# Kernel tuning notes

Measured on AMD Instinct MI355X. Metric: run time of the kernel, lower is better.

The kernel has to match this reference:

```python
import jax, jax.numpy as jnp
import numpy as np

B, T, D, H, HS = 4, 1024, 1024, 16, 64
DW, DA, DG, DV = 64, 64, 128, 32
DM = H * HS  # == D here
EPS = 1e-5
DECAY_C = -0.606531  # -exp(-0.5)


def setup_inputs() -> dict:
    key = jax.random.key(0)
    ks = jax.random.split(key, 24)
    n = lambda k, s: jax.random.normal(k, s, dtype=jnp.float32)
    w = lambda k, s: n(k, s) * (1.0 / np.sqrt(s[0]))
    return dict(
        current=n(ks[0], (B, T, D)),
        prev=n(ks[1], (B, T, D)),
        v_first=n(ks[2], (B, T, DM)),
        rwkvag=jax.random.uniform(ks[3], (6, D), dtype=jnp.float32),
        rw_W=w(ks[4], (D, D)),
        w1=w(ks[5], (D, DW)), w2=w(ks[6], (DW, DM)), w2_b=n(ks[7], (DM,)) * 0.1,
        kw_W=w(ks[8], (D, DM)), vw_W=w(ks[9], (D, DM)),
        a1=w(ks[10], (D, DA)), a2=w(ks[11], (DA, DM)), a2_b=n(ks[12], (DM,)) * 0.1,
        v1=w(ks[13], (D, DV)), v2=w(ks[14], (DV, DM)), v2_b=n(ks[15], (DM,)) * 0.1,
        g1=w(ks[16], (D, DG)), g2=w(ks[17], (DG, DM)), g2_b=n(ks[18], (DM,)) * 0.1,
        k_k=jnp.ones((DM,)), k_a=jax.random.uniform(ks[19], (DM,), dtype=jnp.float32),
        r_k=jnp.ones((DM,)),
        gn_scale=jnp.ones((DM,)), gn_bias=jnp.zeros((DM,)),
        out_W=w(ks[20], (DM, D)),
    )


def _add_heads(x):
    return x.reshape(x.shape[:-1] + (H, HS))


def reference(current, prev, v_first, rwkvag, rw_W, w1, w2, w2_b, kw_W, vw_W,
              a1, a2, a2_b, v1, v2, v2_b, g1, g2, g2_b,
              k_k, k_a, r_k, gn_scale, gn_bias, out_W):
    diff = prev - current
    # per-channel token-shift mixing for the 6 branches: (B,T,6,D)
    x6 = current[..., None, :] + rwkvag * diff[..., None, :]
    xr, xw, xk, xv, xa, xg = (x6[..., i, :] for i in range(6))

    r = xr @ rw_W
    wl = jnp.tanh(xw @ w1) @ w2 + w2_b          # w-LoRA (tanh, bias_post)
    k = xk @ kw_W
    v = xv @ vw_W
    a = jax.nn.sigmoid((xa @ a1) @ a2 + a2_b)   # a-LoRA (bias_post) + sigmoid
    g = jax.nn.sigmoid(xg @ g1) @ g2 + g2_b     # g-LoRA (sigmoid act)

    kk = _add_heads(k * k_k)
    kk = kk / jnp.linalg.norm(kk, axis=-1, keepdims=True)
    k = k * (1.0 + (a - 1.0) * k_a)
    v = v + (v_first - v) * jax.nn.sigmoid((xv @ v1) @ v2 + v2_b)
    wdec = jnp.exp(DECAY_C * jax.nn.sigmoid(wl))  # decay in (exp(-0.6065), 1)

    rk_sum = _add_heads(r * k * r_k).sum(-1, keepdims=True)  # (B,T,H,1)
    rh, wh, kh, vh = _add_heads(r), _add_heads(wdec), _add_heads(k), _add_heads(v)
    at = -kk
    bt = kk * _add_heads(a)

    def step(state, xs):
        rt, wt, ktt, vt, att, btt = xs  # each (B,H,HS)
        sa = jnp.einsum('bhvk,bhk->bhv', state, att)
        state = (state * wt[:, :, None, :]
                 + sa[..., None] * btt[:, :, None, :]
                 + vt[..., None] * ktt[:, :, None, :])
        y = jnp.einsum('bhvk,bhk->bhv', state, rt)
        return state, y

    xs = tuple(jnp.moveaxis(x, 1, 0) for x in (rh, wh, kh, vh, at, bt))
    state0 = jnp.zeros((B, H, HS, HS), dtype=current.dtype)
    state, ys = jax.lax.scan(step, state0, xs)
    out = jnp.moveaxis(ys, 0, 1)  # (B,T,H,HS)

    # GroupNorm with n_head groups (normalize within each head)
    mu = out.mean(-1, keepdims=True)
    var = out.var(-1, keepdims=True)
    outn = (out - mu) * jax.lax.rsqrt(var + EPS)
    outn = outn.reshape(B, T, DM) * gn_scale + gn_bias

    outn = outn + (rk_sum * vh).reshape(B, T, DM)
    y = (outn * g) @ out_W
    return y, state, v_first
```

## Files before the change

### kernel.cpp

```cpp
#include <hip/hip_runtime.h>
#include <math.h>

#define NT 4096
#define DD 1024
#define NH 16
#define HSZ 64
#define GN_EPS 1e-5f
#define DECAY_C -0.606531f

typedef __attribute__((ext_vector_type(8))) short short8;
typedef __attribute__((ext_vector_type(4))) float float4v;

#define GLB(p) ((const __attribute__((address_space(1))) void*)(p))
#define LDS(p) ((__attribute__((address_space(3))) void*)(p))

#define MEMFENCE asm volatile("" ::: "memory")

__device__ __forceinline__ float sigm(float x) { return 1.f / (1.f + __expf(-x)); }

__device__ __forceinline__ unsigned short f2bf(float f) {
    unsigned int u = __float_as_uint(f);
    u = (u + 0x7fffu + ((u >> 16) & 1u)) >> 16;
    return (unsigned short)u;
}
__device__ __forceinline__ float bf2f(unsigned short h) {
    return __uint_as_float(((unsigned int)h) << 16);
}

__device__ __forceinline__ float row_sum16(float x) {
    int t;
    t = __builtin_amdgcn_update_dpp(0, __float_as_int(x), 0x128, 0xF, 0xF, true);
    x += __int_as_float(t);
    t = __builtin_amdgcn_update_dpp(0, __float_as_int(x), 0x124, 0xF, 0xF, true);
    x += __int_as_float(t);
    t = __builtin_amdgcn_update_dpp(0, __float_as_int(x), 0x122, 0xF, 0xF, true);
    x += __int_as_float(t);
    t = __builtin_amdgcn_update_dpp(0, __float_as_int(x), 0x121, 0xF, 0xF, true);
    x += __int_as_float(t);
    return x;
}

__global__ __launch_bounds__(256)
void mix6(const float* __restrict__ cur, const float* __restrict__ prev,
          const float* __restrict__ lam,
          ushort* __restrict__ xrh, ushort* __restrict__ xrl,
          ushort* __restrict__ xwh, ushort* __restrict__ xwl,
          ushort* __restrict__ xkh, ushort* __restrict__ xkl,
          ushort* __restrict__ xvh, ushort* __restrict__ xvl,
          ushort* __restrict__ xah, ushort* __restrict__ xal,
          ushort* __restrict__ xgh, ushort* __restrict__ xgl)
{
    const int tok = blockIdx.x;
    const int d0 = threadIdx.x * 4;
    const size_t base = (size_t)tok * DD + d0;
    float4 c = *(const float4*)(cur + base);
    float4 p = *(const float4*)(prev + base);
    float dx = p.x - c.x, dy = p.y - c.y, dz = p.z - c.z, dw = p.w - c.w;
    ushort* hs[6] = {xrh, xwh, xkh, xvh, xah, xgh};
    ushort* ls[6] = {xrl, xwl, xkl, xvl, xal, xgl};
#pragma unroll
    for (int j = 0; j < 6; j++) {
        float4 l = *(const float4*)(lam + j * DD + d0);
        float m0 = c.x + l.x * dx;
        float m1 = c.y + l.y * dy;
        float m2 = c.z + l.z * dz;
        float m3 = c.w + l.w * dw;
        ushort4 h;
        h.x = f2bf(m0); h.y = f2bf(m1); h.z = f2bf(m2); h.w = f2bf(m3);
        *(ushort4*)(hs[j] + base) = h;
        ushort4 lo;
        lo.x = f2bf(m0 - bf2f(h.x));
        lo.y = f2bf(m1 - bf2f(h.y));
        lo.z = f2bf(m2 - bf2f(h.z));
        lo.w = f2bf(m3 - bf2f(h.w));
        *(ushort4*)(ls[j] + base) = lo;
    }
}

__global__ __launch_bounds__(256)
void transpose_pad(const float* __restrict__ W, ushort* __restrict__ Wh,
                   ushort* __restrict__ Wl, int K, int N)
{
    __shared__ float tile[32][33];
    const int bx = blockIdx.x * 32;
    const int by = blockIdx.y * 32;
    const int tx = threadIdx.x, ty = threadIdx.y;
#pragma unroll
    for (int i = 0; i < 32; i += 8) {
        float v = 0.f;
        if (bx + tx < N) v = W[(size_t)(by + ty + i) * N + bx + tx];
        tile[ty + i][tx] = v;
    }
    __syncthreads();
#pragma unroll
    for (int i = 0; i < 32; i += 8) {
        float v = tile[tx][ty + i];
        ushort h = f2bf(v);
        size_t o = (size_t)(bx + ty + i) * K + by + tx;
        Wh[o] = h;
        if (Wl) Wl[o] = f2bf(v - bf2f(h));
    }
}

#define SWZ(r) (((r) >> 1) & 3)

__global__ __launch_bounds__(256)
void gemm_mega1(const ushort* __restrict__ xrh, const ushort* __restrict__ xrl,
                const ushort* __restrict__ xwh, const ushort* __restrict__ xwl,
                const ushort* __restrict__ xkh, const ushort* __restrict__ xkl,
                const ushort* __restrict__ xvh, const ushort* __restrict__ xvl,
                const ushort* __restrict__ xah, const ushort* __restrict__ xal,
                const ushort* __restrict__ xgh, const ushort* __restrict__ xgl,
                const ushort* __restrict__ Bth, const ushort* __restrict__ Btl,
                float* __restrict__ r_buf, float* __restrict__ k_buf,
                float* __restrict__ v_buf,
                ushort* __restrict__ hwh, ushort* __restrict__ hwl,
                ushort* __restrict__ hah, ushort* __restrict__ hal,
                ushort* __restrict__ hvh, ushort* __restrict__ hvl,
                ushort* __restrict__ hgh, ushort* __restrict__ hgl)
{
    __shared__ ushort As[2][2][128 * 32];
    __shared__ ushort Bs[2][2][128 * 32];
    const int cb = blockIdx.y;
    const ushort* Ah; const ushort* Al;
    if (cb < 8)       { Ah = xrh; Al = xrl; }
    else if (cb < 16) { Ah = xkh; Al = xkl; }
    else if (cb < 24) { Ah = xvh; Al = xvl; }
    else if (cb == 24){ Ah = xwh; Al = xwl; }
    else if (cb == 25){ Ah = xah; Al = xal; }
    else if (cb == 26){ Ah = xvh; Al = xvl; }
    else              { Ah = xgh; Al = xgl; }

    const int tid = threadIdx.x;
    const int rowBase = blockIdx.x * 128;
    const int colBase = cb * 128;
    const int lane = tid & 63;
    const int wave = tid >> 6;
    const int wm = wave >> 1, wn = wave & 1;
    const int m15 = lane & 15, quad = lane >> 4;

    float4v zero4 = {0.f, 0.f, 0.f, 0.f};
    float4v acc[4][4];
#pragma unroll
    for (int i = 0; i < 4; i++)
#pragma unroll
        for (int j = 0; j < 4; j++) acc[i][j] = zero4;

#define STAGE1(kk, bb) do {                                                       \
    const int k0_ = (kk) * 32;                                                    \
    _Pragma("unroll")                                                             \
    for (int i_ = 0; i_ < 2; i_++) {                                              \
        int idx_ = i_ * 256 + tid;                                                \
        int r_ = idx_ >> 2, seg_ = idx_ & 3;                                      \
        int sg_ = seg_ ^ SWZ(r_);       \
        size_t aoff_ = (size_t)(rowBase + r_) * 1024 + k0_ + sg_ * 8;             \
        size_t boff_ = (size_t)(colBase + r_) * 1024 + k0_ + sg_ * 8;             \
        int dst_ = (i_ * 256 + (tid & ~63)) * 8;                                  \
        __builtin_amdgcn_global_load_lds(GLB(Ah + aoff_),  LDS(&As[bb][0][0] + dst_), 16, 0, 0); \
        __builtin_amdgcn_global_load_lds(GLB(Al + aoff_),  LDS(&As[bb][1][0] + dst_), 16, 0, 0); \
        __builtin_amdgcn_global_load_lds(GLB(Bth + boff_), LDS(&Bs[bb][0][0] + dst_), 16, 0, 0); \
        __builtin_amdgcn_global_load_lds(GLB(Btl + boff_), LDS(&Bs[bb][1][0] + dst_), 16, 0, 0); \
    }                                                                             \
} while (0)

    STAGE1(0, 0);
    STAGE1(1, 1);
    asm volatile("s_waitcnt vmcnt(8)" ::: "memory");
    __builtin_amdgcn_s_barrier();
    MEMFENCE;

    for (int kt = 0; kt < 32; kt++) {
        const int buf = kt & 1;

        short8 ah[4], bh[4], al[4], bl[4];
#pragma unroll
        for (int mi = 0; mi < 4; mi++) {
            int ra = wm * 64 + mi * 16 + m15;
            int cs = (quad ^ SWZ(ra)) * 8;
            ah[mi] = *(const short8*)(&As[buf][0][0] + ra * 32 + cs);
            al[mi] = *(const short8*)(&As[buf][1][0] + ra * 32 + cs);
        }
#pragma unroll
        for (int ni = 0; ni < 4; ni++) {
            int rb = wn * 64 + ni * 16 + m15;
            int cs = (quad ^ SWZ(rb)) * 8;
            bh[ni] = *(const short8*)(&Bs[buf][0][0] + rb * 32 + cs);
            bl[ni] = *(const short8*)(&Bs[buf][1][0] + rb * 32 + cs);
        }
#pragma unroll
        for (int mi = 0; mi < 4; mi++)
#pragma unroll
            for (int ni = 0; ni < 4; ni++) {
                acc[mi][ni] = __builtin_amdgcn_mfma_f32_16x16x32_bf16(al[mi], bh[ni], acc[mi][ni], 0, 0, 0);
                acc[mi][ni] = __builtin_amdgcn_mfma_f32_16x16x32_bf16(ah[mi], bl[ni], acc[mi][ni], 0, 0, 0);
                acc[mi][ni] = __builtin_amdgcn_mfma_f32_16x16x32_bf16(ah[mi], bh[ni], acc[mi][ni], 0, 0, 0);
            }

        if (kt == 31) break;

        MEMFENCE;
        __builtin_amdgcn_s_barrier();
        MEMFENCE;
        if (kt < 30) {
            STAGE1(kt + 2, buf);
            asm volatile("s_waitcnt vmcnt(8)" ::: "memory");
        } else {
            asm volatile("s_waitcnt vmcnt(0)" ::: "memory");
        }
        __builtin_amdgcn_s_barrier();
        MEMFENCE;
    }
#undef STAGE1

#pragma unroll
    for (int mi = 0; mi < 4; mi++) {
#pragma unroll
        for (int ni = 0; ni < 4; ni++) {
            int c = wn * 64 + ni * 16 + m15;
#pragma unroll
            for (int rr = 0; rr < 4; rr++) {
                int row = rowBase + wm * 64 + mi * 16 + quad * 4 + rr;
                float v = acc[mi][ni][rr];
                if (cb < 24) {
                    float* dst = (cb < 8) ? r_buf : (cb < 16) ? k_buf : v_buf;
                    int n = (cb & 7) * 128 + c;
                    dst[(size_t)row * 1024 + n] = v;
                } else if (cb == 24) {
                    if (c < 64) {
                        float t = tanhf(v);
                        ushort h = f2bf(t);
                        hwh[(size_t)row * 64 + c] = h;
                        hwl[(size_t)row * 64 + c] = f2bf(t - bf2f(h));
                    }
                } else if (cb == 25) {
                    if (c < 64) {
                        ushort h = f2bf(v);
                        hah[(size_t)row * 64 + c] = h;
                        hal[(size_t)row * 64 + c] = f2bf(v - bf2f(h));
                    }
                } else if (cb == 26) {
                    if (c < 32) {
                        ushort h = f2bf(v);
                        hvh[(size_t)row * 32 + c] = h;
                        hvl[(size_t)row * 32 + c] = f2bf(v - bf2f(h));
                    }
                } else {
                    float t = sigm(v);
                    ushort h = f2bf(t);
                    hgh[(size_t)row * 128 + c] = h;
                    hgl[(size_t)row * 128 + c] = f2bf(t - bf2f(h));
                }
            }
        }
    }
}

__global__ __launch_bounds__(256)
void gemm_mega2(const ushort* __restrict__ hwh, const ushort* __restrict__ hwl,
                const ushort* __restrict__ hah, const ushort* __restrict__ hal,
                const ushort* __restrict__ hvh, const ushort* __restrict__ hvl,
                const ushort* __restrict__ hgh, const ushort* __restrict__ hgl,
                const ushort* __restrict__ w2Th, const ushort* __restrict__ w2Tl,
                const ushort* __restrict__ a2Th, const ushort* __restrict__ a2Tl,
                const ushort* __restrict__ v2Th, const ushort* __restrict__ v2Tl,
                const ushort* __restrict__ g2Th, const ushort* __restrict__ g2Tl,
                const float* __restrict__ w2_b, const float* __restrict__ a2_b,
                const float* __restrict__ v2_b, const float* __restrict__ g2_b,
                float* __restrict__ w_buf, float* __restrict__ a_buf,
                float* __restrict__ vg_buf, float* __restrict__ g_buf)
{
    __shared__ ushort AsH[128 * 32];
    __shared__ ushort BsH[128 * 32];
    __shared__ ushort AsL[128 * 32];
    __shared__ ushort BsL[128 * 32];
    const int cb = blockIdx.y;
    const int seg = cb >> 3;
    const int K = (seg == 2) ? 32 : (seg == 3) ? 128 : 64;
    const ushort *Ah, *Al, *Bh, *Bl;
    const float* bias;
    float* outp;
    if (seg == 0) { Ah = hwh; Al = hwl; Bh = w2Th; Bl = w2Tl; bias = w2_b; outp = w_buf; }
    else if (seg == 1) { Ah = hah; Al = hal; Bh = a2Th; Bl = a2Tl; bias = a2_b; outp = a_buf; }
    else if (seg == 2) { Ah = hvh; Al = hvl; Bh = v2Th; Bl = v2Tl; bias = v2_b; outp = vg_buf; }
    else { Ah = hgh; Al = hgl; Bh = g2Th; Bl = g2Tl; bias = g2_b; outp = g_buf; }

    const int tid = threadIdx.x;
    const int rowBase = blockIdx.x * 128;
    const int colBase = (cb & 7) * 128;
    const int lane = tid & 63;
    const int wave = tid >> 6;
    const int wm = wave >> 1, wn = wave & 1;
    const int m15 = lane & 15, quad = lane >> 4;

    float4v zero4 = {0.f, 0.f, 0.f, 0.f};
    float4v acc[4][4];
#pragma unroll
    for (int i = 0; i < 4; i++)
#pragma unroll
        for (int j = 0; j < 4; j++) acc[i][j] = zero4;

    for (int k0 = 0; k0 < K; k0 += 32) {
#pragma unroll
        for (int i = 0; i < 2; i++) {
            int idx = i * 256 + tid;
            int r = idx >> 2, s8 = idx & 3;
            int sg = s8 ^ SWZ(r);
            size_t aoff = (size_t)(rowBase + r) * K + k0 + sg * 8;
            size_t boff = (size_t)(colBase + r) * K + k0 + sg * 8;
            int dst = (i * 256 + (tid & ~63)) * 8;
            __builtin_amdgcn_global_load_lds(GLB(Ah + aoff), LDS(AsH + dst), 16, 0, 0);
            __builtin_amdgcn_global_load_lds(GLB(Bh + boff), LDS(BsH + dst), 16, 0, 0);
            __builtin_amdgcn_global_load_lds(GLB(Al + aoff), LDS(AsL + dst), 16, 0, 0);
            __builtin_amdgcn_global_load_lds(GLB(Bl + boff), LDS(BsL + dst), 16, 0, 0);
        }
        __syncthreads();
        short8 ah[4], bh[4], al[4], bl[4];
#pragma unroll
        for (int mi = 0; mi < 4; mi++) {
            int ra = wm * 64 + mi * 16 + m15;
            int cs = (quad ^ SWZ(ra)) * 8;
            ah[mi] = *(const short8*)(AsH + ra * 32 + cs);
            al[mi] = *(const short8*)(AsL + ra * 32 + cs);
        }
#pragma unroll
        for (int ni = 0; ni < 4; ni++) {
            int rb = wn * 64 + ni * 16 + m15;
            int cs = (quad ^ SWZ(rb)) * 8;
            bh[ni] = *(const short8*)(BsH + rb * 32 + cs);
            bl[ni] = *(const short8*)(BsL + rb * 32 + cs);
        }
#pragma unroll
        for (int mi = 0; mi < 4; mi++)
#pragma unroll
            for (int ni = 0; ni < 4; ni++) {
                acc[mi][ni] = __builtin_amdgcn_mfma_f32_16x16x32_bf16(al[mi], bh[ni], acc[mi][ni], 0, 0, 0);
                acc[mi][ni] = __builtin_amdgcn_mfma_f32_16x16x32_bf16(ah[mi], bl[ni], acc[mi][ni], 0, 0, 0);
                acc[mi][ni] = __builtin_amdgcn_mfma_f32_16x16x32_bf16(ah[mi], bh[ni], acc[mi][ni], 0, 0, 0);
            }
        __syncthreads();
    }

#pragma unroll
    for (int mi = 0; mi < 4; mi++) {
#pragma unroll
        for (int ni = 0; ni < 4; ni++) {
            int col = colBase + wn * 64 + ni * 16 + m15;
            float bv = bias[col];
#pragma unroll
            for (int rr = 0; rr < 4; rr++) {
                int row = rowBase + wm * 64 + mi * 16 + quad * 4 + rr;
                float v = acc[mi][ni][rr] + bv;
                if (seg == 1 || seg == 2) v = sigm(v);
                outp[(size_t)row * 1024 + col] = v;
            }
        }
    }
}

__global__ __launch_bounds__(256)
void gemm_bf16s(const ushort* __restrict__ Ah, const ushort* __restrict__ Bh,
                float* __restrict__ outF, int N, int K)
{
    __shared__ ushort As2[2][128 * 32];
    __shared__ ushort Bs2[2][128 * 32];
    const int tid = threadIdx.x;
    const int rowBase = blockIdx.x * 128;
    const int colBase = blockIdx.y * 128;
    const int lane = tid & 63;
    const int wave = tid >> 6;
    const int wm = wave >> 1, wn = wave & 1;
    const int m15 = lane & 15, quad = lane >> 4;

    float4v zero4 = {0.f, 0.f, 0.f, 0.f};
    float4v acc[4][4];
#pragma unroll
    for (int i = 0; i < 4; i++)
#pragma unroll
        for (int j = 0; j < 4; j++) acc[i][j] = zero4;

#define STAGE3(kk, bb) do {                                                       \
    const int k0_ = (kk) * 32;                                                    \
    _Pragma("unroll")                                                             \
    for (int i_ = 0; i_ < 2; i_++) {                                              \
        int idx_ = i_ * 256 + tid;                                                \
        int r_ = idx_ >> 2, seg_ = idx_ & 3;                                      \
        int sg_ = seg_ ^ SWZ(r_);                                                 \
        size_t aoff_ = (size_t)(rowBase + r_) * K + k0_ + sg_ * 8;                \
        size_t boff_ = (size_t)(colBase + r_) * K + k0_ + sg_ * 8;                \
        int dst_ = (i_ * 256 + (tid & ~63)) * 8;                                  \
        __builtin_amdgcn_global_load_lds(GLB(Ah + aoff_), LDS(&As2[bb][0] + dst_), 16, 0, 0); \
        __builtin_amdgcn_global_load_lds(GLB(Bh + boff_), LDS(&Bs2[bb][0] + dst_), 16, 0, 0); \
    }                                                                             \
} while (0)

    const int nk = K >> 5;
    STAGE3(0, 0);
    STAGE3(1, 1);
    asm volatile("s_waitcnt vmcnt(4)" ::: "memory");
    __builtin_amdgcn_s_barrier();
    MEMFENCE;

    for (int kt = 0; kt < nk; kt++) {
        const int buf = kt & 1;
        short8 ah[4], bh[4];
#pragma unroll
        for (int mi = 0; mi < 4; mi++) {
            int ra = wm * 64 + mi * 16 + m15;
            ah[mi] = *(const short8*)(&As2[buf][0] + ra * 32 + (quad ^ SWZ(ra)) * 8);
        }
#pragma unroll
        for (int ni = 0; ni < 4; ni++) {
            int rb = wn * 64 + ni * 16 + m15;
            bh[ni] = *(const short8*)(&Bs2[buf][0] + rb * 32 + (quad ^ SWZ(rb)) * 8);
        }
#pragma unroll
        for (int mi = 0; mi < 4; mi++)
#pragma unroll
            for (int ni = 0; ni < 4; ni++)
                acc[mi][ni] = __builtin_amdgcn_mfma_f32_16x16x32_bf16(ah[mi], bh[ni], acc[mi][ni], 0, 0, 0);

        if (kt == nk - 1) break;

        MEMFENCE;
        __builtin_amdgcn_s_barrier();
        MEMFENCE;
        if (kt < nk - 2) {
            STAGE3(kt + 2, buf);
            asm volatile("s_waitcnt vmcnt(4)" ::: "memory");
        } else {
            asm volatile("s_waitcnt vmcnt(0)" ::: "memory");
        }
        __builtin_amdgcn_s_barrier();
        MEMFENCE;
    }
#undef STAGE3

#pragma unroll
    for (int mi = 0; mi < 4; mi++) {
#pragma unroll
        for (int ni = 0; ni < 4; ni++) {
            int col = colBase + wn * 64 + ni * 16 + m15;
#pragma unroll
            for (int rr = 0; rr < 4; rr++) {
                int row = rowBase + wm * 64 + mi * 16 + quad * 4 + rr;
                outF[(size_t)row * N + col] = acc[mi][ni][rr];
            }
        }
    }
}

__global__ __launch_bounds__(256)
void elemwise1(const float* __restrict__ r_buf, float* __restrict__ wl_buf,
               float* __restrict__ k_buf, float* __restrict__ v_buf,
               float* __restrict__ kkn_buf, const float* __restrict__ a_buf,
               const float* __restrict__ vg_buf, const float* __restrict__ vfirst,
               const float* __restrict__ kkw, const float* __restrict__ kaw,
               const float* __restrict__ rkw, float* __restrict__ rk_sum)
{
    const int tok = blockIdx.x;
    const int tid = threadIdx.x;
    const int d0 = tid * 4;
    const size_t base = (size_t)tok * DD + d0;

    float4 k0 = *(const float4*)(k_buf + base);
    float4 a4 = *(const float4*)(a_buf + base);
    float4 wl = *(const float4*)(wl_buf + base);
    float4 v0 = *(const float4*)(v_buf + base);
    float4 vg = *(const float4*)(vg_buf + base);
    float4 vf = *(const float4*)(vfirst + base);
    float4 r4 = *(const float4*)(r_buf + base);
    float4 kkc = *(const float4*)(kkw + d0);
    float4 kac = *(const float4*)(kaw + d0);
    float4 rkc = *(const float4*)(rkw + d0);

    float kk0 = k0.x * kkc.x, kk1 = k0.y * kkc.y, kk2 = k0.z * kkc.z, kk3 = k0.w * kkc.w;
    float ss = kk0 * kk0 + kk1 * kk1 + kk2 * kk2 + kk3 * kk3;
    ss += __shfl_xor(ss, 1); ss += __shfl_xor(ss, 2);
    ss += __shfl_xor(ss, 4); ss += __shfl_xor(ss, 8);
    float rn = rsqrtf(ss);
    float4 kkn = { kk0 * rn, kk1 * rn, kk2 * rn, kk3 * rn };
    *(float4*)(kkn_buf + base) = kkn;

    float4 kf;
    kf.x = k0.x * (1.f + (a4.x - 1.f) * kac.x);
    kf.y = k0.y * (1.f + (a4.y - 1.f) * kac.y);
    kf.z = k0.z * (1.f + (a4.z - 1.f) * kac.z);
    kf.w = k0.w * (1.f + (a4.w - 1.f) * kac.w);
    *(float4*)(k_buf + base) = kf;

    float rk = r4.x * kf.x * rkc.x + r4.y * kf.y * rkc.y + r4.z * kf.z * rkc.z + r4.w * kf.w * rkc.w;
    rk += __shfl_xor(rk, 1); rk += __shfl_xor(rk, 2);
    rk += __shfl_xor(rk, 4); rk += __shfl_xor(rk, 8);
    if ((tid & 15) == 0) rk_sum[(size_t)tok * NH + (tid >> 4)] = rk;

    float4 vfin;
    vfin.x = v0.x + (vf.x - v0.x) * vg.x;
    vfin.y = v0.y + (vf.y - v0.y) * vg.y;
    vfin.z = v0.z + (vf.z - v0.z) * vg.z;
    vfin.w = v0.w + (vf.w - v0.w) * vg.w;
    *(float4*)(v_buf + base) = vfin;

    float4 wd;
    wd.x = __expf(DECAY_C * sigm(wl.x));
    wd.y = __expf(DECAY_C * sigm(wl.y));
    wd.z = __expf(DECAY_C * sigm(wl.z));
    wd.w = __expf(DECAY_C * sigm(wl.w));
    *(float4*)(wl_buf + base) = wd;
}

__global__ __launch_bounds__(256, 1)
void scan_kernel(const float* __restrict__ r_buf, const float* __restrict__ w_buf,
                 const float* __restrict__ k_buf, const float* __restrict__ kkn_buf,
                 const float* __restrict__ a_buf, const float* __restrict__ v_buf,
                 float* __restrict__ out_scan, float* __restrict__ state_out)
{
    __shared__ float vecJ[2][5][16][64];
    __shared__ float vbuf2[2][16][16];
    __shared__ float ypart[2][16][16][20];
    const int bh = blockIdx.x;
    const int rg = blockIdx.y;
    const int b = bh >> 4, h = bh & 15;
    const int tid = threadIdx.x;
    const int row = tid >> 4, l16 = tid & 15;
    const int lofs = l16 * 4;
    const int rowbase = rg * 16;
    const size_t tok0 = ((size_t)b * 1024) * DD + h * HSZ;
    float s0 = 0.f, s1 = 0.f, s2 = 0.f, s3 = 0.f;

#define STAGE(cc, bb) do {                                                        \
    const int tt_ = tid >> 4;                                                     \
    const int dd4_ = (tid & 15) * 4;                                              \
    size_t gofs_ = tok0 + (size_t)((cc) * 16 + tt_) * DD + dd4_;                  \
    float* db_ = &vecJ[bb][0][0][0] + ((tid >> 6) << 8);                          \
    __builtin_amdgcn_global_load_lds(GLB(r_buf + gofs_),   LDS(db_),        16, 0, 0); \
    __builtin_amdgcn_global_load_lds(GLB(w_buf + gofs_),   LDS(db_ + 1024), 16, 0, 0); \
    __builtin_amdgcn_global_load_lds(GLB(k_buf + gofs_),   LDS(db_ + 2048), 16, 0, 0); \
    __builtin_amdgcn_global_load_lds(GLB(kkn_buf + gofs_), LDS(db_ + 3072), 16, 0, 0); \
    __builtin_amdgcn_global_load_lds(GLB(a_buf + gofs_),   LDS(db_ + 4096), 16, 0, 0); \
    if (tid < 64) {                                                               \
        size_t vofs_ = tok0 + (size_t)((cc) * 16 + (tid >> 2)) * DD + rowbase + (tid & 3) * 4; \
        __builtin_amdgcn_global_load_lds(GLB(v_buf + vofs_), LDS(&vbuf2[bb][0][0]), 16, 0, 0); \
    }                                                                             \
} while (0)

#define LD_TOK(P, tt) do {                                                        \
    P##r = *(const float4*)(vb + (tt) * 64 + lofs);                               \
    P##w = *(const float4*)(vb + 1024 + (tt) * 64 + lofs);                        \
    P##k = *(const float4*)(vb + 2048 + (tt) * 64 + lofs);                        \
    P##q = *(const float4*)(vb + 3072 + (tt) * 64 + lofs);                        \
    P##a = *(const float4*)(vb + 4096 + (tt) * 64 + lofs);                        \
    P##v = vbp[(tt) * 16 + row];                                                  \
} while (0)

#define STEP(P, tt) do {                                                          \
    float sa_ = P##q.x * s0;                                                      \
    sa_ = fmaf(P##q.y, s1, sa_);                                                  \
    sa_ = fmaf(P##q.z, s2, sa_);                                                  \
    sa_ = fmaf(P##q.w, s3, sa_);                                                  \
    sa_ = row_sum16(sa_);                                                         \
    float n0_ = P##q.x * P##a.x, n1_ = P##q.y * P##a.y;                           \
    float n2_ = P##q.z * P##a.z, n3_ = P##q.w * P##a.w;                           \
    float b0_ = fmaf(s0, P##w.x, P##v * P##k.x);                                  \
    float b1_ = fmaf(s1, P##w.y, P##v * P##k.y);                                  \
    float b2_ = fmaf(s2, P##w.z, P##v * P##k.z);                                  \
    float b3_ = fmaf(s3, P##w.w, P##v * P##k.w);                                  \
    s0 = fmaf(sa_, -n0_, b0_);                                                    \
    s1 = fmaf(sa_, -n1_, b1_);                                                    \
    s2 = fmaf(sa_, -n2_, b2_);                                                    \
    s3 = fmaf(sa_, -n3_, b3_);                                                    \
    float yp_ = P##r.x * s0;                                                      \
    yp_ = fmaf(P##r.y, s1, yp_);                                                  \
    yp_ = fmaf(P##r.z, s2, yp_);                                                  \
    yp_ = fmaf(P##r.w, s3, yp_);                                                  \
    ypart[buf][tt][row][l16] = yp_;                                               \
} while (0)

    STAGE(0, 0);
    __syncthreads();

    for (int c = 0; c < 64; c++) {
        const int buf = c & 1;
        if (c < 63) STAGE(c + 1, buf ^ 1);
        const float* vb  = &vecJ[buf][0][0][0];
        const float* vbp = &vbuf2[buf][0][0];
        float4 Ar, Aw, Ak, Aq, Aa; float Av;
        float4 Br, Bw, Bk, Bq, Ba; float Bv;
        float4 Cr, Cw, Ck, Cq, Ca; float Cv;
        float4 Dr, Dw, Dk, Dq, Da; float Dv;
        LD_TOK(A, 0); LD_TOK(B, 1); LD_TOK(C, 2);
#pragma unroll
        for (int i4 = 0; i4 < 4; i4++) {
            LD_TOK(D, 4 * i4 + 3);
            STEP(A, 4 * i4);
            if (4 * i4 + 4 < 16) LD_TOK(A, 4 * i4 + 4);
            STEP(B, 4 * i4 + 1);
            if (4 * i4 + 5 < 16) LD_TOK(B, 4 * i4 + 5);
            STEP(C, 4 * i4 + 2);
            if (4 * i4 + 6 < 16) LD_TOK(C, 4 * i4 + 6);
            STEP(D, 4 * i4 + 3);
        }
        __syncthreads();
        {
            const int t_ = tid >> 4, r_ = tid & 15;
            const float* yp = &ypart[buf][t_][r_][0];
            float4 y0 = *(const float4*)(yp);
            float4 y1 = *(const float4*)(yp + 4);
            float4 y2 = *(const float4*)(yp + 8);
            float4 y3 = *(const float4*)(yp + 12);
            float ys = ((y0.x + y0.y) + (y0.z + y0.w)) + ((y1.x + y1.y) + (y1.z + y1.w))
                     + ((y2.x + y2.y) + (y2.z + y2.w)) + ((y3.x + y3.y) + (y3.z + y3.w));
            out_scan[tok0 + (size_t)(c * 16 + t_) * DD + rowbase + r_] = ys;
        }
    }

#undef STAGE
#undef LD_TOK
#undef STEP

    float* so = state_out + ((size_t)(b * NH + h) * HSZ + rowbase + row) * HSZ + l16 * 4;
    float4 sv = {s0, s1, s2, s3};
    *(float4*)so = sv;
}

__global__ __launch_bounds__(256)
void elemwise2(const float* __restrict__ out_scan, const float* __restrict__ rk_sum,
               const float* __restrict__ v_buf, const float* __restrict__ g_buf,
               const float* __restrict__ gscale, const float* __restrict__ gbias,
               ushort* __restrict__ z_buf)
{
    const int tok = blockIdx.x;
    const int tid = threadIdx.x;
    const int d0 = tid * 4;
    const size_t base = (size_t)tok * DD + d0;

    float4 o = *(const float4*)(out_scan + base);
    float sm = o.x + o.y + o.z + o.w;
    float ss = o.x * o.x + o.y * o.y + o.z * o.z + o.w * o.w;
    sm += __shfl_xor(sm, 1); sm += __shfl_xor(sm, 2);
    sm += __shfl_xor(sm, 4); sm += __shfl_xor(sm, 8);
    ss += __shfl_xor(ss, 1); ss += __shfl_xor(ss, 2);
    ss += __shfl_xor(ss, 4); ss += __shfl_xor(ss, 8);
    float mu = sm * (1.f / 64.f);
    float var = ss * (1.f / 64.f) - mu * mu;
    float rs = rsqrtf(var + GN_EPS);
    float rk = rk_sum[(size_t)tok * NH + (tid >> 4)];

    float4 v4 = *(const float4*)(v_buf + base);
    float4 g4 = *(const float4*)(g_buf + base);
    float4 gs = *(const float4*)(gscale + d0);
    float4 gb = *(const float4*)(gbias + d0);
    ushort4 z;
    z.x = f2bf(((o.x - mu) * rs * gs.x + gb.x + rk * v4.x) * g4.x);
    z.y = f2bf(((o.y - mu) * rs * gs.y + gb.y + rk * v4.y) * g4.y);
    z.z = f2bf(((o.z - mu) * rs * gs.z + gb.z + rk * v4.z) * g4.z);
    z.w = f2bf(((o.w - mu) * rs * gs.w + gb.w + rk * v4.w) * g4.w);
    *(ushort4*)(z_buf + base) = z;
}

extern "C" void kernel_launch(void* const* d_in, const int* in_sizes, int n_in,
                              void* d_out, int out_size, void* d_ws, size_t ws_size,
                              hipStream_t stream) {
    const float* cur    = (const float*)d_in[0];
    const float* prev   = (const float*)d_in[1];
    const float* vfirst = (const float*)d_in[2];
    const float* rwkvag = (const float*)d_in[3];
    const float* rw_W   = (const float*)d_in[4];
    const float* w1     = (const float*)d_in[5];
    const float* w2     = (const float*)d_in[6];
    const float* w2_b   = (const float*)d_in[7];
    const float* kw_W   = (const float*)d_in[8];
    const float* vw_W   = (const float*)d_in[9];
    const float* a1     = (const float*)d_in[10];
    const float* a2     = (const float*)d_in[11];
    const float* a2_b   = (const float*)d_in[12];
    const float* v1     = (const float*)d_in[13];
    const float* v2     = (const float*)d_in[14];
    const float* v2_b   = (const float*)d_in[15];
    const float* g1     = (const float*)d_in[16];
    const float* g2     = (const float*)d_in[17];
    const float* g2_b   = (const float*)d_in[18];
    const float* k_k    = (const float*)d_in[19];
    const float* k_a    = (const float*)d_in[20];
    const float* r_k    = (const float*)d_in[21];
    const float* gn_s   = (const float*)d_in[22];
    const float* gn_b   = (const float*)d_in[23];
    const float* out_W  = (const float*)d_in[24];

    float* out = (float*)d_out;
    float* y_out = out;
    float* state_out = out + (size_t)NT * DD;
    float* vf_out = state_out + (size_t)4 * NH * HSZ * HSZ;

    float* p = (float*)d_ws;
    const size_t big = (size_t)NT * DD;
    const size_t half = big / 2;
    float* r_buf = p;   p += big;
    float* k_buf = p;   p += big;
    float* v_buf = p;   p += big;
    float* xreg = p;
    ushort* xrh = (ushort*)(xreg);            ushort* xrl = (ushort*)(xreg + half);
    ushort* xwh = (ushort*)(xreg + 2*half);   ushort* xwl = (ushort*)(xreg + 3*half);
    ushort* xkh = (ushort*)(xreg + 4*half);   ushort* xkl = (ushort*)(xreg + 5*half);
    ushort* xvh = (ushort*)(xreg + 6*half);   ushort* xvl = (ushort*)(xreg + 7*half);
    ushort* xah = (ushort*)(xreg + 8*half);   ushort* xal = (ushort*)(xreg + 9*half);
    ushort* xgh = (ushort*)(xreg + 10*half);  ushort* xgl = (ushort*)(xreg + 11*half);
    p += 12 * half;
    float* w_buf   = xreg + 0 * half;
    float* a_buf   = xreg + 2 * half;
    float* vg_buf  = xreg + 4 * half;
    float* os_buf  = vg_buf;
    float* g_buf   = xreg + 6 * half;
    float* kkn_buf = xreg + 8 * half;
    float* btreg = p;
    ushort* Bth = (ushort*)btreg;
    ushort* Btl = (ushort*)(btreg + 1835008);
    p += 2 * 1835008;
    ushort* z_bf  = (ushort*)btreg;
    ushort* outTh = (ushort*)(btreg + 2097152);
    ushort* w2Th = (ushort*)p; p += 32768; ushort* w2Tl = (ushort*)p; p += 32768;
    ushort* a2Th = (ushort*)p; p += 32768; ushort* a2Tl = (ushort*)p; p += 32768;
    ushort* v2Th = (ushort*)p; p += 16384; ushort* v2Tl = (ushort*)p; p += 16384;
    ushort* g2Th = (ushort*)p; p += 65536; ushort* g2Tl = (ushort*)p; p += 65536;
    ushort* hwh = (ushort*)p; p += 131072; ushort* hwl = (ushort*)p; p += 131072;
    ushort* hah = (ushort*)p; p += 131072; ushort* hal = (ushort*)p; p += 131072;
    ushort* hvh = (ushort*)p; p += 65536;  ushort* hvl = (ushort*)p; p += 65536;
    ushort* hgh = (ushort*)p; p += 262144; ushort* hgl = (ushort*)p; p += 262144;
    float* rks_buf = p;        p += 65536;

    dim3 blk(256);
    dim3 t32x8(32, 8);

    transpose_pad<<<dim3(32, 32), t32x8, 0, stream>>>(rw_W, Bth + (size_t)0 * 1024,    Btl + (size_t)0 * 1024,    1024, 1024);
    transpose_pad<<<dim3(32, 32), t32x8, 0, stream>>>(kw_W, Bth + (size_t)1024 * 1024, Btl + (size_t)1024 * 1024, 1024, 1024);
    transpose_pad<<<dim3(32, 32), t32x8, 0, stream>>>(vw_W, Bth + (size_t)2048 * 1024, Btl + (size_t)2048 * 1024, 1024, 1024);
    transpose_pad<<<dim3(4, 32), t32x8, 0, stream>>>(w1, Bth + (size_t)3072 * 1024, Btl + (size_t)3072 * 1024, 1024, 64);
    transpose_pad<<<dim3(4, 32), t32x8, 0, stream>>>(a1, Bth + (size_t)3200 * 1024, Btl + (size_t)3200 * 1024, 1024, 64);
    transpose_pad<<<dim3(4, 32), t32x8, 0, stream>>>(v1, Bth + (size_t)3328 * 1024, Btl + (size_t)3328 * 1024, 1024, 32);
    transpose_pad<<<dim3(4, 32), t32x8, 0, stream>>>(g1, Bth + (size_t)3456 * 1024, Btl + (size_t)3456 * 1024, 1024, 128);
    transpose_pad<<<dim3(32, 2), t32x8, 0, stream>>>(w2, w2Th, w2Tl, 64, 1024);
    transpose_pad<<<dim3(32, 2), t32x8, 0, stream>>>(a2, a2Th, a2Tl, 64, 1024);
    transpose_pad<<<dim3(32, 1), t32x8, 0, stream>>>(v2, v2Th, v2Tl, 32, 1024);
    transpose_pad<<<dim3(32, 4), t32x8, 0, stream>>>(g2, g2Th, g2Tl, 128, 1024);

    mix6<<<NT, blk, 0, stream>>>(cur, prev, rwkvag,
                                 xrh, xrl, xwh, xwl, xkh, xkl,
                                 xvh, xvl, xah, xal, xgh, xgl);

    gemm_mega1<<<dim3(32, 28), blk, 0, stream>>>(
        xrh, xrl, xwh, xwl, xkh, xkl, xvh, xvl, xah, xal, xgh, xgl,
        Bth, Btl, r_buf, k_buf, v_buf,
        hwh, hwl, hah, hal, hvh, hvl, hgh, hgl);

    transpose_pad<<<dim3(32, 32), t32x8, 0, stream>>>(out_W, outTh, nullptr, 1024, 1024);

    gemm_mega2<<<dim3(32, 32), blk, 0, stream>>>(
        hwh, hwl, hah, hal, hvh, hvl, hgh, hgl,
        w2Th, w2Tl, a2Th, a2Tl, v2Th, v2Tl, g2Th, g2Tl,
        w2_b, a2_b, v2_b, g2_b,
        w_buf, a_buf, vg_buf, g_buf);

    elemwise1<<<NT, blk, 0, stream>>>(r_buf, w_buf, k_buf, v_buf, kkn_buf, a_buf,
                                      vg_buf, vfirst, k_k, k_a, r_k, rks_buf);

    scan_kernel<<<dim3(64, 4), blk, 0, stream>>>(r_buf, w_buf, k_buf, kkn_buf, a_buf, v_buf,
                                                 os_buf, state_out);

    elemwise2<<<NT, blk, 0, stream>>>(os_buf, rks_buf, v_buf, g_buf, gn_s, gn_b, z_bf);

    gemm_bf16s<<<dim3(32, 8), blk, 0, stream>>>(z_bf, outTh, y_out, 1024, 1024);

    hipMemcpyAsync(vf_out, vfirst, (size_t)NT * DD * sizeof(float),
                   hipMemcpyDeviceToDevice, stream);
}
```

Measured before the change: 523.2 us.

## Widen scan blocks to 32 state rows and precompute kk*a in elemwise

The scan kernel now runs 512 threads per block, each block covering 32 state rows of a head, so the grid halves and each token's vectors are staged once per 32 rows instead of 16. The per-row y reduction moves from an LDS partial buffer plus a post-sync pass to an in-register row_sum16 with a direct store. The kk*a product is precomputed in elemwise1 and overwrites a_buf, which removes multiplies from the serial recurrence. The token prefetch pipeline shrinks from four to two registers sets, and writes to out_scan become scattered single-lane stores.

```diff
diff --git a/kernel.cpp b/kernel.cpp
--- a/kernel.cpp
+++ b/kernel.cpp
@@ -452,7 +452,7 @@
 __global__ __launch_bounds__(256)
 void elemwise1(const float* __restrict__ r_buf, float* __restrict__ wl_buf,
                float* __restrict__ k_buf, float* __restrict__ v_buf,
-               float* __restrict__ kkn_buf, const float* __restrict__ a_buf,
+               float* __restrict__ kkn_buf, float* __restrict__ a_buf,
                const float* __restrict__ vg_buf, const float* __restrict__ vfirst,
                const float* __restrict__ kkw, const float* __restrict__ kaw,
                const float* __restrict__ rkw, float* __restrict__ rk_sum)
@@ -481,6 +481,9 @@
     float4 kkn = { kk0 * rn, kk1 * rn, kk2 * rn, kk3 * rn };
     *(float4*)(kkn_buf + base) = kkn;
 
+    float4 nbt = { kkn.x * a4.x, kkn.y * a4.y, kkn.z * a4.z, kkn.w * a4.w };
+    *(float4*)(a_buf + base) = nbt;
+
     float4 kf;
     kf.x = k0.x * (1.f + (a4.x - 1.f) * kac.x);
     kf.y = k0.y * (1.f + (a4.y - 1.f) * kac.y);
@@ -508,38 +511,41 @@
     *(float4*)(wl_buf + base) = wd;
 }
 
-__global__ __launch_bounds__(256, 1)
+__global__ __launch_bounds__(512, 1)
 void scan_kernel(const float* __restrict__ r_buf, const float* __restrict__ w_buf,
                  const float* __restrict__ k_buf, const float* __restrict__ kkn_buf,
                  const float* __restrict__ a_buf, const float* __restrict__ v_buf,
                  float* __restrict__ out_scan, float* __restrict__ state_out)
 {
     __shared__ float vecJ[2][5][16][64];
-    __shared__ float vbuf2[2][16][16];
-    __shared__ float ypart[2][16][16][20];
+    __shared__ float vbuf2[2][16][32];
     const int bh = blockIdx.x;
     const int rg = blockIdx.y;
     const int b = bh >> 4, h = bh & 15;
     const int tid = threadIdx.x;
-    const int row = tid >> 4, l16 = tid & 15;
+    const int row = tid >> 4;
+    const int l16 = tid & 15;
     const int lofs = l16 * 4;
-    const int rowbase = rg * 16;
+    const int rowbase = rg * 32;
     const size_t tok0 = ((size_t)b * 1024) * DD + h * HSZ;
     float s0 = 0.f, s1 = 0.f, s2 = 0.f, s3 = 0.f;
 
 #define STAGE(cc, bb) do {                                                        \
-    const int tt_ = tid >> 4;                                                     \
-    const int dd4_ = (tid & 15) * 4;                                              \
-    size_t gofs_ = tok0 + (size_t)((cc) * 16 + tt_) * DD + dd4_;                  \
-    float* db_ = &vecJ[bb][0][0][0] + ((tid >> 6) << 8);                          \
-    __builtin_amdgcn_global_load_lds(GLB(r_buf + gofs_),   LDS(db_),        16, 0, 0); \
-    __builtin_amdgcn_global_load_lds(GLB(w_buf + gofs_),   LDS(db_ + 1024), 16, 0, 0); \
-    __builtin_amdgcn_global_load_lds(GLB(k_buf + gofs_),   LDS(db_ + 2048), 16, 0, 0); \
-    __builtin_amdgcn_global_load_lds(GLB(kkn_buf + gofs_), LDS(db_ + 3072), 16, 0, 0); \
-    __builtin_amdgcn_global_load_lds(GLB(a_buf + gofs_),   LDS(db_ + 4096), 16, 0, 0); \
-    if (tid < 64) {                                                               \
-        size_t vofs_ = tok0 + (size_t)((cc) * 16 + (tid >> 2)) * DD + rowbase + (tid & 3) * 4; \
-        __builtin_amdgcn_global_load_lds(GLB(v_buf + vofs_), LDS(&vbuf2[bb][0][0]), 16, 0, 0); \
+    if (tid < 256) {                                                              \
+        const int tt_ = tid >> 4;                                                 \
+        const int dd4_ = (tid & 15) * 4;                                          \
+        size_t gofs_ = tok0 + (size_t)((cc) * 16 + tt_) * DD + dd4_;              \
+        float* db_ = &vecJ[bb][0][0][0] + ((tid >> 6) << 8);                      \
+        __builtin_amdgcn_global_load_lds(GLB(r_buf + gofs_),   LDS(db_),        16, 0, 0); \
+        __builtin_amdgcn_global_load_lds(GLB(w_buf + gofs_),   LDS(db_ + 1024), 16, 0, 0); \
+        __builtin_amdgcn_global_load_lds(GLB(k_buf + gofs_),   LDS(db_ + 2048), 16, 0, 0); \
+        __builtin_amdgcn_global_load_lds(GLB(kkn_buf + gofs_), LDS(db_ + 3072), 16, 0, 0); \
+        __builtin_amdgcn_global_load_lds(GLB(a_buf + gofs_),   LDS(db_ + 4096), 16, 0, 0); \
+    }                                                                             \
+    if (tid < 128) {                                                              \
+        size_t vofs_ = tok0 + (size_t)((cc) * 16 + (tid >> 3)) * DD + rowbase + (tid & 7) * 4; \
+        float* vd_ = &vbuf2[bb][0][0] + ((tid >> 6) << 8);                        \
+        __builtin_amdgcn_global_load_lds(GLB(v_buf + vofs_), LDS(vd_), 16, 0, 0); \
     }                                                                             \
 } while (0)
 
@@ -549,7 +555,7 @@
     P##k = *(const float4*)(vb + 2048 + (tt) * 64 + lofs);                        \
     P##q = *(const float4*)(vb + 3072 + (tt) * 64 + lofs);                        \
     P##a = *(const float4*)(vb + 4096 + (tt) * 64 + lofs);                        \
-    P##v = vbp[(tt) * 16 + row];                                                  \
+    P##v = vbp[(tt) * 32 + row];                                                  \
 } while (0)
 
 #define STEP(P, tt) do {                                                          \
@@ -558,21 +564,21 @@
     sa_ = fmaf(P##q.z, s2, sa_);                                                  \
     sa_ = fmaf(P##q.w, s3, sa_);                                                  \
     sa_ = row_sum16(sa_);                                                         \
-    float n0_ = P##q.x * P##a.x, n1_ = P##q.y * P##a.y;                           \
-    float n2_ = P##q.z * P##a.z, n3_ = P##q.w * P##a.w;                           \
     float b0_ = fmaf(s0, P##w.x, P##v * P##k.x);                                  \
     float b1_ = fmaf(s1, P##w.y, P##v * P##k.y);                                  \
     float b2_ = fmaf(s2, P##w.z, P##v * P##k.z);                                  \
     float b3_ = fmaf(s3, P##w.w, P##v * P##k.w);                                  \
-    s0 = fmaf(sa_, -n0_, b0_);                                                    \
-    s1 = fmaf(sa_, -n1_, b1_);                                                    \
-    s2 = fmaf(sa_, -n2_, b2_);                                                    \
-    s3 = fmaf(sa_, -n3_, b3_);                                                    \
-    float yp_ = P##r.x * s0;                                                      \
-    yp_ = fmaf(P##r.y, s1, yp_);                                                  \
-    yp_ = fmaf(P##r.z, s2, yp_);                                                  \
-    yp_ = fmaf(P##r.w, s3, yp_);                                                  \
-    ypart[buf][tt][row][l16] = yp_;                                               \
+    s0 = fmaf(sa_, -P##a.x, b0_);                                                 \
+    s1 = fmaf(sa_, -P##a.y, b1_);                                                 \
+    s2 = fmaf(sa_, -P##a.z, b2_);                                                 \
+    s3 = fmaf(sa_, -P##a.w, b3_);                                                 \
+    float y_ = P##r.x * s0;                                                       \
+    y_ = fmaf(P##r.y, s1, y_);                                                    \
+    y_ = fmaf(P##r.z, s2, y_);                                                    \
+    y_ = fmaf(P##r.w, s3, y_);                                                    \
+    y_ = row_sum16(y_);                                                           \
+    if (l16 == 0)                                                                 \
+        out_scan[tok0 + (size_t)((c) * 16 + (tt)) * DD + rowbase + row] = y_;     \
 } while (0)
 
     STAGE(0, 0);
@@ -585,32 +591,15 @@
         const float* vbp = &vbuf2[buf][0][0];
         float4 Ar, Aw, Ak, Aq, Aa; float Av;
         float4 Br, Bw, Bk, Bq, Ba; float Bv;
-        float4 Cr, Cw, Ck, Cq, Ca; float Cv;
-        float4 Dr, Dw, Dk, Dq, Da; float Dv;
-        LD_TOK(A, 0); LD_TOK(B, 1); LD_TOK(C, 2);
-#pragma unroll
-        for (int i4 = 0; i4 < 4; i4++) {
-            LD_TOK(D, 4 * i4 + 3);
-            STEP(A, 4 * i4);
-            if (4 * i4 + 4 < 16) LD_TOK(A, 4 * i4 + 4);
-            STEP(B, 4 * i4 + 1);
-            if (4 * i4 + 5 < 16) LD_TOK(B, 4 * i4 + 5);
-            STEP(C, 4 * i4 + 2);
-            if (4 * i4 + 6 < 16) LD_TOK(C, 4 * i4 + 6);
-            STEP(D, 4 * i4 + 3);
+        LD_TOK(A, 0);
+#pragma unroll
+        for (int tp = 0; tp < 8; tp++) {
+            LD_TOK(B, 2 * tp + 1);
+            STEP(A, 2 * tp);
+            if (tp < 7) LD_TOK(A, 2 * tp + 2);
+            STEP(B, 2 * tp + 1);
         }
         __syncthreads();
-        {
-            const int t_ = tid >> 4, r_ = tid & 15;
-            const float* yp = &ypart[buf][t_][r_][0];
-            float4 y0 = *(const float4*)(yp);
-            float4 y1 = *(const float4*)(yp + 4);
-            float4 y2 = *(const float4*)(yp + 8);
-            float4 y3 = *(const float4*)(yp + 12);
-            float ys = ((y0.x + y0.y) + (y0.z + y0.w)) + ((y1.x + y1.y) + (y1.z + y1.w))
-                     + ((y2.x + y2.y) + (y2.z + y2.w)) + ((y3.x + y3.y) + (y3.z + y3.w));
-            out_scan[tok0 + (size_t)(c * 16 + t_) * DD + rowbase + r_] = ys;
-        }
     }
 
 #undef STAGE
@@ -762,8 +751,8 @@
     elemwise1<<<NT, blk, 0, stream>>>(r_buf, w_buf, k_buf, v_buf, kkn_buf, a_buf,
                                       vg_buf, vfirst, k_k, k_a, r_k, rks_buf);
 
-    scan_kernel<<<dim3(64, 4), blk, 0, stream>>>(r_buf, w_buf, k_buf, kkn_buf, a_buf, v_buf,
-                                                 os_buf, state_out);
+    scan_kernel<<<dim3(64, 2), dim3(512), 0, stream>>>(r_buf, w_buf, k_buf, kkn_buf, a_buf, v_buf,
+                                                       os_buf, state_out);
 
     elemwise2<<<NT, blk, 0, stream>>>(os_buf, rks_buf, v_buf, g_buf, gn_s, gn_b, z_bf);
 
```

After: 555.6 us. +6.2%, slower.
